# Performance work log

Hardware: AMD Instinct MI355X
Metric: run time of the kernel (lower is better)

## Reference

```python
import jax, jax.numpy as jnp
import numpy as np

K = 6  # number of deformation subdivision steps
LEVEL = 5  # icosphere subdivision level -> 10242 verts, 20480 faces
EPS = 1e-12


def _icosphere(level):
    t = (1.0 + 5.0 ** 0.5) / 2.0
    verts = np.array([
        [-1, t, 0], [1, t, 0], [-1, -t, 0], [1, -t, 0],
        [0, -1, t], [0, 1, t], [0, -1, -t], [0, 1, -t],
        [t, 0, -1], [t, 0, 1], [-t, 0, -1], [-t, 0, 1]], dtype=np.float64)
    verts /= np.linalg.norm(verts, axis=1, keepdims=True)
    faces = [[0, 11, 5], [0, 5, 1], [0, 1, 7], [0, 7, 10], [0, 10, 11],
             [1, 5, 9], [5, 11, 4], [11, 10, 2], [10, 7, 6], [7, 1, 8],
             [3, 9, 4], [3, 4, 2], [3, 2, 6], [3, 6, 8], [3, 8, 9],
             [4, 9, 5], [2, 4, 11], [6, 2, 10], [8, 6, 7], [9, 8, 1]]
    for _ in range(level):
        vlist = [v for v in verts]
        cache = {}
        def mid(a, b):
            key = (min(a, b), max(a, b))
            if key not in cache:
                m = vlist[a] + vlist[b]
                m = m / np.linalg.norm(m)
                vlist.append(m)
                cache[key] = len(vlist) - 1
            return cache[key]
        new_faces = []
        for a, b, c in faces:
            ab, bc, ca = mid(a, b), mid(b, c), mid(c, a)
            new_faces += [[a, ab, ca], [b, bc, ab], [c, ca, bc], [ab, bc, ca]]
        faces = new_faces
        verts = np.stack(vlist)
    return verts.astype(np.float32), np.asarray(faces, dtype=np.int32)


def _norm(a):
    return a / jnp.maximum(jnp.linalg.norm(a, axis=-1, keepdims=True), EPS)


def setup_inputs() -> dict:
    key = jax.random.key(0)
    v_np, f_np = _icosphere(LEVEL)  # [10242,3], [20480,3]
    x = jax.random.normal(key, (v_np.shape[0], 6), dtype=jnp.float32)
    return {"x": x, "v": jnp.asarray(v_np), "f": jnp.asarray(f_np)}


def _forward(x, v, f):
    # Build rotation frame from the 6D feature
    rot_x = _norm(x[..., :3])
    rot_z = _norm(jnp.cross(rot_x, x[..., 3:]))
    rot_y = _norm(jnp.cross(rot_z, rot_x))
    # Axis-angle of the rotation matrix with rows (rot_x, rot_y, rot_z)
    axis = jnp.concatenate([
        rot_y[..., 2:3] - rot_z[..., 1:2],
        rot_z[..., 0:1] - rot_x[..., 2:3],
        rot_x[..., 1:2] - rot_y[..., 0:1]], axis=-1)
    trace = (rot_x[..., 0:1] + rot_y[..., 1:2] + rot_z[..., 2:3] - 1.0) * 0.5
    trace = jnp.clip(trace, -1.0 + 1e-7, 1.0 - 1e-7)
    angle = -jnp.arccos(trace) / (2 ** K)
    axis = _norm(axis)
    # Rodrigues rotation of mesh vertices by angle/2^k about per-point axis
    dot = jnp.sum(axis * v, axis=-1, keepdims=True)
    cross = jnp.cross(axis, v)
    cos, sin = jnp.cos(angle), jnp.sin(angle)
    p = v * cos + cross * sin + axis * (dot * (1.0 - cos))  # [N,3]
    # Nearest-triangle search data: face centers on the sphere
    centers = _norm(v[f].mean(axis=1))  # [F,3]
    for _ in range(K):
        p = _norm(p)
        # Nearest face by center direction; [N,F] score matrix (memory-bound)
        fid = jnp.argmax(p @ centers.T, axis=-1)  # [N]
        tri = v[f[fid]]  # [N,3,3] gathered triangle vertices
        # Gnomonic barycentric coords: solve [v0 v1 v2] b = p, normalize
        b = jnp.linalg.solve(jnp.swapaxes(tri, -1, -2), p[..., None])[..., 0]
        bary = b / jnp.sum(b, axis=-1, keepdims=True)  # [N,3]
        # Barycentric gather-interpolate of current point field
        p = jnp.sum(p[f[fid]] * bary[..., None], axis=-2)  # [N,3]
    return _norm(p)


def reference(x, v, f):
    return _forward(x, v, f)
```

## Files before the change

kernel.cpp:

```cpp
#include <hip/hip_runtime.h>
#include <hip/hip_bf16.h>
#include <math.h>

#define EPSN 1e-12f
#define MARGIN 0.02f

__global__ __launch_bounds__(256)
void centers_kernel(const int* __restrict__ f,
                    const float* __restrict__ v,
                    float4* __restrict__ fine4,
                    int F)
{
    int i = blockIdx.x * 256 + threadIdx.x;
    if (i >= F) return;
    int a = f[i * 3 + 0], b = f[i * 3 + 1], c = f[i * 3 + 2];
    float mx = (v[a * 3 + 0] + v[b * 3 + 0] + v[c * 3 + 0]) * (1.0f / 3.0f);
    float my = (v[a * 3 + 1] + v[b * 3 + 1] + v[c * 3 + 1]) * (1.0f / 3.0f);
    float mz = (v[a * 3 + 2] + v[b * 3 + 2] + v[c * 3 + 2]) * (1.0f / 3.0f);
    float r = 1.0f / fmaxf(sqrtf(mx * mx + my * my + mz * mz), EPSN);
    fine4[i] = make_float4(mx * r, my * r, mz * r, 0.0f);
}

__global__ __launch_bounds__(256)
void coarse_kernel(const float4* __restrict__ fine4,
                   float4* __restrict__ coarse4,
                   int C)
{
    int t = blockIdx.x * 256 + threadIdx.x;
    int c = t >> 6, lane = t & 63;
    if (c >= C) return;
    float4 fc = fine4[(c << 6) + lane];
    float sx = fc.x, sy = fc.y, sz = fc.z;
    for (int off = 32; off >= 1; off >>= 1) {
        sx += __shfl_xor(sx, off);
        sy += __shfl_xor(sy, off);
        sz += __shfl_xor(sz, off);
    }
    if (lane == 0) {
        float r = 1.0f / fmaxf(sqrtf(sx * sx + sy * sy + sz * sz), EPSN);
        coarse4[c] = make_float4(sx * r, sy * r, sz * r, 0.0f);
    }
}

__global__ __launch_bounds__(256)
void init_kernel(const float* __restrict__ x,
                 const float* __restrict__ v,
                 float4* __restrict__ v4,
                 float4* __restrict__ p0,
                 int N)
{
    int n = blockIdx.x * 256 + threadIdx.x;
    if (n >= N) return;

    float ax = x[n * 6 + 0], ay = x[n * 6 + 1], az = x[n * 6 + 2];
    float bx = x[n * 6 + 3], by = x[n * 6 + 4], bz = x[n * 6 + 5];

    float l = fmaxf(sqrtf(ax * ax + ay * ay + az * az), EPSN);
    float rxx = ax / l, rxy = ay / l, rxz = az / l;
    float czx = rxy * bz - rxz * by;
    float czy = rxz * bx - rxx * bz;
    float czz = rxx * by - rxy * bx;
    l = fmaxf(sqrtf(czx * czx + czy * czy + czz * czz), EPSN);
    float rzx = czx / l, rzy = czy / l, rzz = czz / l;
    float cyx = rzy * rxz - rzz * rxy;
    float cyy = rzz * rxx - rzx * rxz;
    float cyz = rzx * rxy - rzy * rxx;
    l = fmaxf(sqrtf(cyx * cyx + cyy * cyy + cyz * cyz), EPSN);
    float ryx = cyx / l, ryy = cyy / l, ryz = cyz / l;

    float axx = ryz - rzy;
    float axy = rzx - rxz;
    float axz = rxy - ryx;
    float trace = (rxx + ryy + rzz - 1.0f) * 0.5f;
    trace = fminf(fmaxf(trace, -1.0f + 1e-7f), 1.0f - 1e-7f);
    float angle = -acosf(trace) * (1.0f / 64.0f);
    l = fmaxf(sqrtf(axx * axx + axy * axy + axz * axz), EPSN);
    axx /= l; axy /= l; axz /= l;

    float vx = v[n * 3 + 0], vy = v[n * 3 + 1], vz = v[n * 3 + 2];
    float d = axx * vx + axy * vy + axz * vz;
    float crx = axy * vz - axz * vy;
    float cry = axz * vx - axx * vz;
    float crz = axx * vy - axy * vx;
    float s, c;
    sincosf(angle, &s, &c);
    float omc = 1.0f - c;
    p0[n] = make_float4(vx * c + crx * s + axx * (d * omc),
                        vy * c + cry * s + axy * (d * omc),
                        vz * c + crz * s + axz * (d * omc), 0.0f);
    v4[n] = make_float4(vx, vy, vz, 0.0f);
}

__global__ __launch_bounds__(256)
void iter_kernel(const float4* __restrict__ pin,
                 float4* __restrict__ pout,
                 const float4* __restrict__ fine4,
                 const float4* __restrict__ coarse4,
                 const int* __restrict__ f,
                 const float4* __restrict__ v4,
                 float* __restrict__ out_final,
                 int N)
{
    const int tid  = threadIdx.x;
    const int wave = tid >> 6;
    const int lane = tid & 63;
    const int pt   = blockIdx.x * 4 + wave;
    if (pt >= N) return;

    float4 p = pin[pt];
    float rl = 1.0f / fmaxf(sqrtf(p.x * p.x + p.y * p.y + p.z * p.z), EPSN);
    float pnx = p.x * rl, pny = p.y * rl, pnz = p.z * rl;

    float4 c0 = coarse4[lane];
    float4 c1 = coarse4[lane + 64];
    float4 c2 = coarse4[lane + 128];
    float4 c3 = coarse4[lane + 192];
    float4 c4 = coarse4[lane + 256];
    float s0 = pnx * c0.x + pny * c0.y + pnz * c0.z;
    float s1 = pnx * c1.x + pny * c1.y + pnz * c1.z;
    float s2 = pnx * c2.x + pny * c2.y + pnz * c2.z;
    float s3 = pnx * c3.x + pny * c3.y + pnz * c3.z;
    float s4 = pnx * c4.x + pny * c4.y + pnz * c4.z;

    float bs = fmaxf(fmaxf(fmaxf(s0, s1), fmaxf(s2, s3)), s4);
    for (int off = 32; off >= 1; off >>= 1)
        bs = fmaxf(bs, __shfl_xor(bs, off));
    const float thr = bs - MARGIN;

    float best = -1e30f;
    int bidx = 0;
    unsigned long long m;
    #define EXPAND(CC)                                                        \
        {                                                                     \
            int cand = ((CC) << 6) + lane;                                    \
            float4 fc = fine4[cand];                                          \
            float sc = pnx * fc.x + pny * fc.y + pnz * fc.z;                  \
            if (sc > best) { best = sc; bidx = cand; }                        \
        }
    m = __ballot(s0 >= thr);
    while (m) { int src = __ffsll(m) - 1; m &= m - 1; EXPAND(src); }
    m = __ballot(s1 >= thr);
    while (m) { int src = __ffsll(m) - 1; m &= m - 1; EXPAND(src + 64); }
    m = __ballot(s2 >= thr);
    while (m) { int src = __ffsll(m) - 1; m &= m - 1; EXPAND(src + 128); }
    m = __ballot(s3 >= thr);
    while (m) { int src = __ffsll(m) - 1; m &= m - 1; EXPAND(src + 192); }
    m = __ballot(s4 >= thr);
    while (m) { int src = __ffsll(m) - 1; m &= m - 1; EXPAND(src + 256); }
    #undef EXPAND

    for (int off = 32; off >= 1; off >>= 1) {
        float sx = __shfl_xor(best, off);
        int   ix = __shfl_xor(bidx, off);
        if (sx > best || (sx == best && ix < bidx)) { best = sx; bidx = ix; }
    }

    if (lane == 0) {
        int i0 = f[bidx * 3 + 0];
        int i1 = f[bidx * 3 + 1];
        int i2 = f[bidx * 3 + 2];
        float4 A = v4[i0];
        float4 B = v4[i1];
        float4 C = v4[i2];

        float bcx = B.y * C.z - B.z * C.y;
        float bcy = B.z * C.x - B.x * C.z;
        float bcz = B.x * C.y - B.y * C.x;
        float D0 = pnx * bcx + pny * bcy + pnz * bcz;
        float pcx = pny * C.z - pnz * C.y;
        float pcy = pnz * C.x - pnx * C.z;
        float pcz = pnx * C.y - pny * C.x;
        float D1 = A.x * pcx + A.y * pcy + A.z * pcz;
        float bpx = B.y * pnz - B.z * pny;
        float bpy = B.z * pnx - B.x * pnz;
        float bpz = B.x * pny - B.y * pnx;
        float D2 = A.x * bpx + A.y * bpy + A.z * bpz;

        float inv = 1.0f / (D0 + D1 + D2);
        float w0 = D0 * inv, w1 = D1 * inv, w2 = D2 * inv;

        float4 q0 = pin[i0];
        float4 q1 = pin[i1];
        float4 q2 = pin[i2];
        float r0 = 1.0f / fmaxf(sqrtf(q0.x * q0.x + q0.y * q0.y + q0.z * q0.z), EPSN);
        float r1 = 1.0f / fmaxf(sqrtf(q1.x * q1.x + q1.y * q1.y + q1.z * q1.z), EPSN);
        float r2 = 1.0f / fmaxf(sqrtf(q2.x * q2.x + q2.y * q2.y + q2.z * q2.z), EPSN);

        float ox = w0 * q0.x * r0 + w1 * q1.x * r1 + w2 * q2.x * r2;
        float oy = w0 * q0.y * r0 + w1 * q1.y * r1 + w2 * q2.y * r2;
        float oz = w0 * q0.z * r0 + w1 * q1.z * r1 + w2 * q2.z * r2;

        if (out_final) {
            float r = 1.0f / fmaxf(sqrtf(ox * ox + oy * oy + oz * oz), EPSN);
            out_final[pt * 3 + 0] = ox * r;
            out_final[pt * 3 + 1] = oy * r;
            out_final[pt * 3 + 2] = oz * r;
        } else {
            pout[pt] = make_float4(ox, oy, oz, 0.0f);
        }
    }
}

extern "C" void kernel_launch(void* const* d_in, const int* in_sizes, int n_in,
                              void* d_out, int out_size, void* d_ws, size_t ws_size,
                              hipStream_t stream)
{
    const float* x = (const float*)d_in[0];
    const float* v = (const float*)d_in[1];
    const int*   f = (const int*)d_in[2];
    float* out = (float*)d_out;

    const int N = in_sizes[1] / 3;
    const int F = in_sizes[2] / 3;
    const int C = F >> 6;

    char* ws = (char*)d_ws;
    size_t off = 0;
    float4* fine4   = (float4*)(ws + off); off += (size_t)F * sizeof(float4);
    float4* coarse4 = (float4*)(ws + off); off += (size_t)C * sizeof(float4);
    float4* v4      = (float4*)(ws + off); off += (size_t)N * sizeof(float4);
    float4* p0      = (float4*)(ws + off); off += (size_t)N * sizeof(float4);
    float4* p1      = (float4*)(ws + off);

    centers_kernel<<<(F + 255) / 256, 256, 0, stream>>>(f, v, fine4, F);
    coarse_kernel<<<(C * 64 + 255) / 256, 256, 0, stream>>>(fine4, coarse4, C);
    init_kernel<<<(N + 255) / 256, 256, 0, stream>>>(x, v, v4, p0, N);

    const int blocks = (N + 3) / 4;
    float4* pin = p0;
    float4* pout = p1;
    for (int k = 0; k < 6; ++k) {
        bool last = (k == 5);
        iter_kernel<<<blocks, 256, 0, stream>>>(
            pin, pout, fine4, coarse4, f, v4, last ? out : nullptr, N);
        float4* t = pin; pin = pout; pout = t;
    }
}
```

Baseline: 128.1 us.

## Fuse all stages into one persistent kernel with software grid barriers

Replaces the nine separate launches (centers, coarse, init, six iterations) with a single persistent kernel of 256 blocks of 1024 threads that synchronises via atomic-counter grid barriers. Center and coarse computation are also fused into one wave-level pass. This removes per-launch overhead and inter-kernel gaps, and hoists the coarse-center loads out of the per-point loop. In exchange it relies on all 256 blocks being co-resident to avoid deadlock, and spin barriers plus fewer waves per point loop may reduce latency hiding.

```diff
diff --git a/kernel.cpp b/kernel.cpp
--- a/kernel.cpp
+++ b/kernel.cpp
@@ -4,200 +4,214 @@
 
 #define EPSN 1e-12f
 #define MARGIN 0.02f
-
-__global__ __launch_bounds__(256)
-void centers_kernel(const int* __restrict__ f,
+#define NBLK 256
+#define NTHR 1024
+
+__global__ void zero_kernel(int* __restrict__ bar)
+{
+    if (threadIdx.x < 16) bar[threadIdx.x] = 0;
+}
+
+__device__ __forceinline__ void grid_barrier(int* bar, int idx)
+{
+    __syncthreads();
+    if (threadIdx.x == 0) {
+        __threadfence();
+        atomicAdd(&bar[idx], 1);
+        while (__hip_atomic_load(&bar[idx], __ATOMIC_RELAXED,
+                                 __HIP_MEMORY_SCOPE_AGENT) < NBLK)
+            __builtin_amdgcn_s_sleep(2);
+        __threadfence();
+    }
+    __syncthreads();
+}
+
+__global__ __launch_bounds__(NTHR)
+void persist_kernel(const float* __restrict__ x,
                     const float* __restrict__ v,
+                    const int* __restrict__ f,
                     float4* __restrict__ fine4,
-                    int F)
-{
-    int i = blockIdx.x * 256 + threadIdx.x;
-    if (i >= F) return;
-    int a = f[i * 3 + 0], b = f[i * 3 + 1], c = f[i * 3 + 2];
-    float mx = (v[a * 3 + 0] + v[b * 3 + 0] + v[c * 3 + 0]) * (1.0f / 3.0f);
-    float my = (v[a * 3 + 1] + v[b * 3 + 1] + v[c * 3 + 1]) * (1.0f / 3.0f);
-    float mz = (v[a * 3 + 2] + v[b * 3 + 2] + v[c * 3 + 2]) * (1.0f / 3.0f);
-    float r = 1.0f / fmaxf(sqrtf(mx * mx + my * my + mz * mz), EPSN);
-    fine4[i] = make_float4(mx * r, my * r, mz * r, 0.0f);
-}
-
-__global__ __launch_bounds__(256)
-void coarse_kernel(const float4* __restrict__ fine4,
-                   float4* __restrict__ coarse4,
-                   int C)
-{
-    int t = blockIdx.x * 256 + threadIdx.x;
-    int c = t >> 6, lane = t & 63;
-    if (c >= C) return;
-    float4 fc = fine4[(c << 6) + lane];
-    float sx = fc.x, sy = fc.y, sz = fc.z;
-    for (int off = 32; off >= 1; off >>= 1) {
-        sx += __shfl_xor(sx, off);
-        sy += __shfl_xor(sy, off);
-        sz += __shfl_xor(sz, off);
-    }
-    if (lane == 0) {
-        float r = 1.0f / fmaxf(sqrtf(sx * sx + sy * sy + sz * sz), EPSN);
-        coarse4[c] = make_float4(sx * r, sy * r, sz * r, 0.0f);
-    }
-}
-
-__global__ __launch_bounds__(256)
-void init_kernel(const float* __restrict__ x,
-                 const float* __restrict__ v,
-                 float4* __restrict__ v4,
-                 float4* __restrict__ p0,
-                 int N)
-{
-    int n = blockIdx.x * 256 + threadIdx.x;
-    if (n >= N) return;
-
-    float ax = x[n * 6 + 0], ay = x[n * 6 + 1], az = x[n * 6 + 2];
-    float bx = x[n * 6 + 3], by = x[n * 6 + 4], bz = x[n * 6 + 5];
-
-    float l = fmaxf(sqrtf(ax * ax + ay * ay + az * az), EPSN);
-    float rxx = ax / l, rxy = ay / l, rxz = az / l;
-    float czx = rxy * bz - rxz * by;
-    float czy = rxz * bx - rxx * bz;
-    float czz = rxx * by - rxy * bx;
-    l = fmaxf(sqrtf(czx * czx + czy * czy + czz * czz), EPSN);
-    float rzx = czx / l, rzy = czy / l, rzz = czz / l;
-    float cyx = rzy * rxz - rzz * rxy;
-    float cyy = rzz * rxx - rzx * rxz;
-    float cyz = rzx * rxy - rzy * rxx;
-    l = fmaxf(sqrtf(cyx * cyx + cyy * cyy + cyz * cyz), EPSN);
-    float ryx = cyx / l, ryy = cyy / l, ryz = cyz / l;
-
-    float axx = ryz - rzy;
-    float axy = rzx - rxz;
-    float axz = rxy - ryx;
-    float trace = (rxx + ryy + rzz - 1.0f) * 0.5f;
-    trace = fminf(fmaxf(trace, -1.0f + 1e-7f), 1.0f - 1e-7f);
-    float angle = -acosf(trace) * (1.0f / 64.0f);
-    l = fmaxf(sqrtf(axx * axx + axy * axy + axz * axz), EPSN);
-    axx /= l; axy /= l; axz /= l;
-
-    float vx = v[n * 3 + 0], vy = v[n * 3 + 1], vz = v[n * 3 + 2];
-    float d = axx * vx + axy * vy + axz * vz;
-    float crx = axy * vz - axz * vy;
-    float cry = axz * vx - axx * vz;
-    float crz = axx * vy - axy * vx;
-    float s, c;
-    sincosf(angle, &s, &c);
-    float omc = 1.0f - c;
-    p0[n] = make_float4(vx * c + crx * s + axx * (d * omc),
-                        vy * c + cry * s + axy * (d * omc),
-                        vz * c + crz * s + axz * (d * omc), 0.0f);
-    v4[n] = make_float4(vx, vy, vz, 0.0f);
-}
-
-__global__ __launch_bounds__(256)
-void iter_kernel(const float4* __restrict__ pin,
-                 float4* __restrict__ pout,
-                 const float4* __restrict__ fine4,
-                 const float4* __restrict__ coarse4,
-                 const int* __restrict__ f,
-                 const float4* __restrict__ v4,
-                 float* __restrict__ out_final,
-                 int N)
+                    float4* __restrict__ coarse4,
+                    float4* __restrict__ v4,
+                    float4* __restrict__ pA,
+                    float4* __restrict__ pB,
+                    float* __restrict__ out,
+                    int* __restrict__ bar,
+                    int N, int F)
 {
     const int tid  = threadIdx.x;
-    const int wave = tid >> 6;
     const int lane = tid & 63;
-    const int pt   = blockIdx.x * 4 + wave;
-    if (pt >= N) return;
-
-    float4 p = pin[pt];
-    float rl = 1.0f / fmaxf(sqrtf(p.x * p.x + p.y * p.y + p.z * p.z), EPSN);
-    float pnx = p.x * rl, pny = p.y * rl, pnz = p.z * rl;
+    const int t    = blockIdx.x * NTHR + tid;
+    const int gw   = t >> 6;
+    const int NW   = (NBLK * NTHR) >> 6;
+    const int C    = F >> 6;
+
+    if (gw < C) {
+        int fi = (gw << 6) + lane;
+        int a = f[fi * 3 + 0], b = f[fi * 3 + 1], c = f[fi * 3 + 2];
+        float mx = v[a * 3 + 0] + v[b * 3 + 0] + v[c * 3 + 0];
+        float my = v[a * 3 + 1] + v[b * 3 + 1] + v[c * 3 + 1];
+        float mz = v[a * 3 + 2] + v[b * 3 + 2] + v[c * 3 + 2];
+        float r = 1.0f / fmaxf(sqrtf(mx * mx + my * my + mz * mz), EPSN);
+        float fx = mx * r, fy = my * r, fz = mz * r;
+        fine4[fi] = make_float4(fx, fy, fz, 0.0f);
+        float sx = fx, sy = fy, sz = fz;
+        for (int off = 32; off >= 1; off >>= 1) {
+            sx += __shfl_xor(sx, off);
+            sy += __shfl_xor(sy, off);
+            sz += __shfl_xor(sz, off);
+        }
+        if (lane == 0) {
+            float rr = 1.0f / fmaxf(sqrtf(sx * sx + sy * sy + sz * sz), EPSN);
+            coarse4[gw] = make_float4(sx * rr, sy * rr, sz * rr, 0.0f);
+        }
+    }
+
+    if (t < N) {
+        float ax = x[t * 6 + 0], ay = x[t * 6 + 1], az = x[t * 6 + 2];
+        float bx = x[t * 6 + 3], by = x[t * 6 + 4], bz = x[t * 6 + 5];
+
+        float l = fmaxf(sqrtf(ax * ax + ay * ay + az * az), EPSN);
+        float rxx = ax / l, rxy = ay / l, rxz = az / l;
+        float czx = rxy * bz - rxz * by;
+        float czy = rxz * bx - rxx * bz;
+        float czz = rxx * by - rxy * bx;
+        l = fmaxf(sqrtf(czx * czx + czy * czy + czz * czz), EPSN);
+        float rzx = czx / l, rzy = czy / l, rzz = czz / l;
+        float cyx = rzy * rxz - rzz * rxy;
+        float cyy = rzz * rxx - rzx * rxz;
+        float cyz = rzx * rxy - rzy * rxx;
+        l = fmaxf(sqrtf(cyx * cyx + cyy * cyy + cyz * cyz), EPSN);
+        float ryx = cyx / l, ryy = cyy / l, ryz = cyz / l;
+
+        float axx = ryz - rzy;
+        float axy = rzx - rxz;
+        float axz = rxy - ryx;
+        float trace = (rxx + ryy + rzz - 1.0f) * 0.5f;
+        trace = fminf(fmaxf(trace, -1.0f + 1e-7f), 1.0f - 1e-7f);
+        float angle = -acosf(trace) * (1.0f / 64.0f);
+        l = fmaxf(sqrtf(axx * axx + axy * axy + axz * axz), EPSN);
+        axx /= l; axy /= l; axz /= l;
+
+        float vx = v[t * 3 + 0], vy = v[t * 3 + 1], vz = v[t * 3 + 2];
+        float d = axx * vx + axy * vy + axz * vz;
+        float crx = axy * vz - axz * vy;
+        float cry = axz * vx - axx * vz;
+        float crz = axx * vy - axy * vx;
+        float s, c;
+        sincosf(angle, &s, &c);
+        float omc = 1.0f - c;
+        pA[t] = make_float4(vx * c + crx * s + axx * (d * omc),
+                            vy * c + cry * s + axy * (d * omc),
+                            vz * c + crz * s + axz * (d * omc), 0.0f);
+        v4[t] = make_float4(vx, vy, vz, 0.0f);
+    }
+
+    grid_barrier(bar, 0);
 
     float4 c0 = coarse4[lane];
     float4 c1 = coarse4[lane + 64];
     float4 c2 = coarse4[lane + 128];
     float4 c3 = coarse4[lane + 192];
     float4 c4 = coarse4[lane + 256];
-    float s0 = pnx * c0.x + pny * c0.y + pnz * c0.z;
-    float s1 = pnx * c1.x + pny * c1.y + pnz * c1.z;
-    float s2 = pnx * c2.x + pny * c2.y + pnz * c2.z;
-    float s3 = pnx * c3.x + pny * c3.y + pnz * c3.z;
-    float s4 = pnx * c4.x + pny * c4.y + pnz * c4.z;
-
-    float bs = fmaxf(fmaxf(fmaxf(s0, s1), fmaxf(s2, s3)), s4);
-    for (int off = 32; off >= 1; off >>= 1)
-        bs = fmaxf(bs, __shfl_xor(bs, off));
-    const float thr = bs - MARGIN;
-
-    float best = -1e30f;
-    int bidx = 0;
-    unsigned long long m;
-    #define EXPAND(CC)                                                        \
-        {                                                                     \
-            int cand = ((CC) << 6) + lane;                                    \
-            float4 fc = fine4[cand];                                          \
-            float sc = pnx * fc.x + pny * fc.y + pnz * fc.z;                  \
-            if (sc > best) { best = sc; bidx = cand; }                        \
+
+    const float4* pin = pA;
+    float4* pout = pB;
+
+    #pragma unroll 1
+    for (int k = 0; k < 6; ++k) {
+        const bool last = (k == 5);
+        for (int pt = gw; pt < N; pt += NW) {
+            float4 p = pin[pt];
+            float rl = 1.0f / fmaxf(sqrtf(p.x * p.x + p.y * p.y + p.z * p.z), EPSN);
+            float pnx = p.x * rl, pny = p.y * rl, pnz = p.z * rl;
+
+            float s0 = pnx * c0.x + pny * c0.y + pnz * c0.z;
+            float s1 = pnx * c1.x + pny * c1.y + pnz * c1.z;
+            float s2 = pnx * c2.x + pny * c2.y + pnz * c2.z;
+            float s3 = pnx * c3.x + pny * c3.y + pnz * c3.z;
+            float s4 = pnx * c4.x + pny * c4.y + pnz * c4.z;
+
+            float bs = fmaxf(fmaxf(fmaxf(s0, s1), fmaxf(s2, s3)), s4);
+            for (int off = 32; off >= 1; off >>= 1)
+                bs = fmaxf(bs, __shfl_xor(bs, off));
+            const float thr = bs - MARGIN;
+
+            float best = -1e30f;
+            int bidx = 0;
+            unsigned long long m;
+            #define EXPAND(CC)                                                \
+                {                                                             \
+                    int cand = ((CC) << 6) + lane;                            \
+                    float4 fc = fine4[cand];                                  \
+                    float sc = pnx * fc.x + pny * fc.y + pnz * fc.z;          \
+                    if (sc > best) { best = sc; bidx = cand; }                \
+                }
+            m = __ballot(s0 >= thr);
+            while (m) { int src = __ffsll(m) - 1; m &= m - 1; EXPAND(src); }
+            m = __ballot(s1 >= thr);
+            while (m) { int src = __ffsll(m) - 1; m &= m - 1; EXPAND(src + 64); }
+            m = __ballot(s2 >= thr);
+            while (m) { int src = __ffsll(m) - 1; m &= m - 1; EXPAND(src + 128); }
+            m = __ballot(s3 >= thr);
+            while (m) { int src = __ffsll(m) - 1; m &= m - 1; EXPAND(src + 192); }
+            m = __ballot(s4 >= thr);
+            while (m) { int src = __ffsll(m) - 1; m &= m - 1; EXPAND(src + 256); }
+            #undef EXPAND
+
+            for (int off = 32; off >= 1; off >>= 1) {
+                float sx2 = __shfl_xor(best, off);
+                int   ix2 = __shfl_xor(bidx, off);
+                if (sx2 > best || (sx2 == best && ix2 < bidx)) { best = sx2; bidx = ix2; }
+            }
+
+            if (lane == 0) {
+                int i0 = f[bidx * 3 + 0];
+                int i1 = f[bidx * 3 + 1];
+                int i2 = f[bidx * 3 + 2];
+                float4 A = v4[i0];
+                float4 B = v4[i1];
+                float4 Cv = v4[i2];
+                float4 q0 = pin[i0];
+                float4 q1 = pin[i1];
+                float4 q2 = pin[i2];
+
+                float bcx = B.y * Cv.z - B.z * Cv.y;
+                float bcy = B.z * Cv.x - B.x * Cv.z;
+                float bcz = B.x * Cv.y - B.y * Cv.x;
+                float D0 = pnx * bcx + pny * bcy + pnz * bcz;
+                float pcx = pny * Cv.z - pnz * Cv.y;
+                float pcy = pnz * Cv.x - pnx * Cv.z;
+                float pcz = pnx * Cv.y - pny * Cv.x;
+                float D1 = A.x * pcx + A.y * pcy + A.z * pcz;
+                float bpx = B.y * pnz - B.z * pny;
+                float bpy = B.z * pnx - B.x * pnz;
+                float bpz = B.x * pny - B.y * pnx;
+                float D2 = A.x * bpx + A.y * bpy + A.z * bpz;
+
+                float inv = 1.0f / (D0 + D1 + D2);
+                float w0 = D0 * inv, w1 = D1 * inv, w2 = D2 * inv;
+
+                float r0 = 1.0f / fmaxf(sqrtf(q0.x * q0.x + q0.y * q0.y + q0.z * q0.z), EPSN);
+                float r1 = 1.0f / fmaxf(sqrtf(q1.x * q1.x + q1.y * q1.y + q1.z * q1.z), EPSN);
+                float r2 = 1.0f / fmaxf(sqrtf(q2.x * q2.x + q2.y * q2.y + q2.z * q2.z), EPSN);
+
+                float ox = w0 * q0.x * r0 + w1 * q1.x * r1 + w2 * q2.x * r2;
+                float oy = w0 * q0.y * r0 + w1 * q1.y * r1 + w2 * q2.y * r2;
+                float oz = w0 * q0.z * r0 + w1 * q1.z * r1 + w2 * q2.z * r2;
+
+                if (last) {
+                    float r = 1.0f / fmaxf(sqrtf(ox * ox + oy * oy + oz * oz), EPSN);
+                    out[pt * 3 + 0] = ox * r;
+                    out[pt * 3 + 1] = oy * r;
+                    out[pt * 3 + 2] = oz * r;
+                } else {
+                    pout[pt] = make_float4(ox, oy, oz, 0.0f);
+                }
+            }
         }
-    m = __ballot(s0 >= thr);
-    while (m) { int src = __ffsll(m) - 1; m &= m - 1; EXPAND(src); }
-    m = __ballot(s1 >= thr);
-    while (m) { int src = __ffsll(m) - 1; m &= m - 1; EXPAND(src + 64); }
-    m = __ballot(s2 >= thr);
-    while (m) { int src = __ffsll(m) - 1; m &= m - 1; EXPAND(src + 128); }
-    m = __ballot(s3 >= thr);
-    while (m) { int src = __ffsll(m) - 1; m &= m - 1; EXPAND(src + 192); }
-    m = __ballot(s4 >= thr);
-    while (m) { int src = __ffsll(m) - 1; m &= m - 1; EXPAND(src + 256); }
-    #undef EXPAND
-
-    for (int off = 32; off >= 1; off >>= 1) {
-        float sx = __shfl_xor(best, off);
-        int   ix = __shfl_xor(bidx, off);
-        if (sx > best || (sx == best && ix < bidx)) { best = sx; bidx = ix; }
-    }
-
-    if (lane == 0) {
-        int i0 = f[bidx * 3 + 0];
-        int i1 = f[bidx * 3 + 1];
-        int i2 = f[bidx * 3 + 2];
-        float4 A = v4[i0];
-        float4 B = v4[i1];
-        float4 C = v4[i2];
-
-        float bcx = B.y * C.z - B.z * C.y;
-        float bcy = B.z * C.x - B.x * C.z;
-        float bcz = B.x * C.y - B.y * C.x;
-        float D0 = pnx * bcx + pny * bcy + pnz * bcz;
-        float pcx = pny * C.z - pnz * C.y;
-        float pcy = pnz * C.x - pnx * C.z;
-        float pcz = pnx * C.y - pny * C.x;
-        float D1 = A.x * pcx + A.y * pcy + A.z * pcz;
-        float bpx = B.y * pnz - B.z * pny;
-        float bpy = B.z * pnx - B.x * pnz;
-        float bpz = B.x * pny - B.y * pnx;
-        float D2 = A.x * bpx + A.y * bpy + A.z * bpz;
-
-        float inv = 1.0f / (D0 + D1 + D2);
-        float w0 = D0 * inv, w1 = D1 * inv, w2 = D2 * inv;
-
-        float4 q0 = pin[i0];
-        float4 q1 = pin[i1];
-        float4 q2 = pin[i2];
-        float r0 = 1.0f / fmaxf(sqrtf(q0.x * q0.x + q0.y * q0.y + q0.z * q0.z), EPSN);
-        float r1 = 1.0f / fmaxf(sqrtf(q1.x * q1.x + q1.y * q1.y + q1.z * q1.z), EPSN);
-        float r2 = 1.0f / fmaxf(sqrtf(q2.x * q2.x + q2.y * q2.y + q2.z * q2.z), EPSN);
-
-        float ox = w0 * q0.x * r0 + w1 * q1.x * r1 + w2 * q2.x * r2;
-        float oy = w0 * q0.y * r0 + w1 * q1.y * r1 + w2 * q2.y * r2;
-        float oz = w0 * q0.z * r0 + w1 * q1.z * r1 + w2 * q2.z * r2;
-
-        if (out_final) {
-            float r = 1.0f / fmaxf(sqrtf(ox * ox + oy * oy + oz * oz), EPSN);
-            out_final[pt * 3 + 0] = ox * r;
-            out_final[pt * 3 + 1] = oy * r;
-            out_final[pt * 3 + 2] = oz * r;
-        } else {
-            pout[pt] = make_float4(ox, oy, oz, 0.0f);
-        }
+        if (!last) grid_barrier(bar, k + 1);
+        const float4* tp = pin; pin = pout; pout = (float4*)tp;
     }
 }
 
@@ -210,29 +224,20 @@
     const int*   f = (const int*)d_in[2];
     float* out = (float*)d_out;
 
-    const int N = in_sizes[1] / 3;
-    const int F = in_sizes[2] / 3;
+    int N = in_sizes[1] / 3;
+    int F = in_sizes[2] / 3;
     const int C = F >> 6;
 
     char* ws = (char*)d_ws;
-    size_t off = 0;
+    int* bar = (int*)ws;
+    size_t off = 256;
     float4* fine4   = (float4*)(ws + off); off += (size_t)F * sizeof(float4);
     float4* coarse4 = (float4*)(ws + off); off += (size_t)C * sizeof(float4);
     float4* v4      = (float4*)(ws + off); off += (size_t)N * sizeof(float4);
     float4* p0      = (float4*)(ws + off); off += (size_t)N * sizeof(float4);
     float4* p1      = (float4*)(ws + off);
 
-    centers_kernel<<<(F + 255) / 256, 256, 0, stream>>>(f, v, fine4, F);
-    coarse_kernel<<<(C * 64 + 255) / 256, 256, 0, stream>>>(fine4, coarse4, C);
-    init_kernel<<<(N + 255) / 256, 256, 0, stream>>>(x, v, v4, p0, N);
-
-    const int blocks = (N + 3) / 4;
-    float4* pin = p0;
-    float4* pout = p1;
-    for (int k = 0; k < 6; ++k) {
-        bool last = (k == 5);
-        iter_kernel<<<blocks, 256, 0, stream>>>(
-            pin, pout, fine4, coarse4, f, v4, last ? out : nullptr, N);
-        float4* t = pin; pin = pout; pout = t;
-    }
-}
+    zero_kernel<<<1, 64, 0, stream>>>(bar);
+    persist_kernel<<<NBLK, NTHR, 0, stream>>>(
+        x, v, f, fine4, coarse4, v4, p0, p1, out, bar, N, F);
+}
```

New measurement: 250.5 us. 1.96x slower.
